# Kernel tuning notes

Hardware: AMD Instinct MI355X
Metric: run time of the kernel (lower is better)

## Reference

```python
import jax, jax.numpy as jnp
import numpy as np

B, L, DIM, H = 4, 2048, 768, 12
C = DIM // H  # head_dim = 64


def setup_inputs() -> dict:
    key = jax.random.key(0)
    k1, k2, k3 = jax.random.split(key, 3)
    x = jax.random.normal(k1, (B, L, DIM), dtype=jnp.float32)
    # qkv Linear: torch uniform init +-sqrt(6/(dim + 3*dim... per code: out//3 + in))
    val_qkv = np.sqrt(6.0 / float(DIM + DIM))
    Wqkv = jax.random.uniform(k2, (DIM, 3 * DIM), dtype=jnp.float32,
                              minval=-val_qkv, maxval=val_qkv)  # [in, out]
    # proj_out Linear: xavier uniform, bias zeros
    val_o = np.sqrt(6.0 / float(DIM + DIM))
    Wo = jax.random.uniform(k3, (DIM, DIM), dtype=jnp.float32,
                            minval=-val_o, maxval=val_o)  # [in, out]
    bo = jnp.zeros((DIM,), dtype=jnp.float32)
    return {"x": x, "Wqkv": Wqkv, "Wo": Wo, "bo": bo}


def reference(x, Wqkv, Wo, bo):
    b, l, d = x.shape
    qkv = x @ Wqkv                                   # [B, L, 3*dim] (qkv_bias=False)
    qkv = qkv.reshape(b, l, 3, H, C)                 # three interleaved as (three H C)
    q, k, v = qkv[:, :, 0], qkv[:, :, 1], qkv[:, :, 2]  # each [B, L, H, C]
    # NOTE: original forward never applies self.scale -> unscaled dot products
    dots = jnp.einsum('bqhc,bkhc->bhqk', q, k)       # [B, H, L, L]
    attn = jax.nn.softmax(dots, axis=-1)             # attn_drop = 0 -> identity
    out = jnp.einsum('bhqk,bkhc->bqhc', attn, v)     # [B, L, H, C]
    out = out.reshape(b, l, d)                       # (H C) -> dim
    return out @ Wo + bo                             # proj_drop = 0 -> identity
```

## Files before the change

kernel.cpp:

```cpp
#include <hip/hip_runtime.h>
#include <hip/hip_bf16.h>


typedef unsigned short u16;
typedef u16 u16x2 __attribute__((ext_vector_type(2)));
typedef u16 u16x4 __attribute__((ext_vector_type(4)));
typedef u16 u16x8 __attribute__((ext_vector_type(8)));
typedef short bf16x8 __attribute__((ext_vector_type(8)));
typedef float f32x4 __attribute__((ext_vector_type(4)));

#define MFMA16(acc, a, b) \
  asm("v_mfma_f32_16x16x32_bf16 %0, %1, %2, %0" : "+v"(acc) : "v"(a), "v"(b))

__device__ __forceinline__ u16 f2b(float f) {
  unsigned u = __float_as_uint(f);
  return (u16)((u + 0x7fffu + ((u >> 16) & 1u)) >> 16);
}
__device__ __forceinline__ float b2f(u16 h) {
  return __uint_as_float(((unsigned)h) << 16);
}
__device__ __forceinline__ unsigned pk_bf16(float a, float b) {
  unsigned d;
  asm("v_cvt_pk_bf16_f32 %0, %1, %2" : "=v"(d) : "v"(a), "v"(b));
  return d;
}

__device__ __forceinline__ void gload16(const u16* g, u16* l) {
  __builtin_amdgcn_global_load_lds(
      (const __attribute__((address_space(1))) unsigned*)g,
      (__attribute__((address_space(3))) unsigned*)l, 16, 0, 0);
}

__global__ __launch_bounds__(256) void prep_x_kernel(
    const float* __restrict__ X, u16* __restrict__ Xh, u16* __restrict__ Xl) {
  const size_t i = ((size_t)blockIdx.x * 256 + threadIdx.x) * 4;
  float4 v = *(const float4*)(X + i);
  u16 h0 = f2b(v.x), h1 = f2b(v.y), h2 = f2b(v.z), h3 = f2b(v.w);
  u16x4 hs = { h0, h1, h2, h3 };
  u16x4 ls = { f2b(v.x - b2f(h0)), f2b(v.y - b2f(h1)),
               f2b(v.z - b2f(h2)), f2b(v.w - b2f(h3)) };
  *(u16x4*)(Xh + i) = hs;
  *(u16x4*)(Xl + i) = ls;
}

__global__ __launch_bounds__(256) void prep_w_kernel(
    const float* __restrict__ W, u16* __restrict__ WtH, u16* __restrict__ WtL,
    int K, int N) {
  __shared__ float T[32][33];
  const int k0 = blockIdx.x * 32, n0 = blockIdx.y * 32;
  const int tx = threadIdx.x & 31, ty = threadIdx.x >> 5;
  #pragma unroll
  for (int i = 0; i < 4; ++i)
    T[ty + i * 8][tx] = W[(size_t)(k0 + ty + i * 8) * N + n0 + tx];
  __syncthreads();
  #pragma unroll
  for (int i = 0; i < 4; ++i) {
    const int rn = ty + i * 8, ck = tx;
    float v = T[ck][rn];
    u16 h = f2b(v);
    WtH[(size_t)(n0 + rn) * K + k0 + ck] = h;
    WtL[(size_t)(n0 + rn) * K + k0 + ck] = f2b(v - b2f(h));
  }
}

__global__ __launch_bounds__(256) void prep_wo_kernel(
    const float* __restrict__ W, u16* __restrict__ Wt, int K, int N) {
  __shared__ float T[32][33];
  const int k0 = blockIdx.x * 32, n0 = blockIdx.y * 32;
  const int tx = threadIdx.x & 31, ty = threadIdx.x >> 5;
  #pragma unroll
  for (int i = 0; i < 4; ++i)
    T[ty + i * 8][tx] = W[(size_t)(k0 + ty + i * 8) * N + n0 + tx];
  __syncthreads();
  #pragma unroll
  for (int i = 0; i < 4; ++i) {
    const int rn = ty + i * 8, ck = tx;
    Wt[(size_t)(n0 + rn) * K + k0 + ck] = f2b(T[ck][rn]);
  }
}

__global__ __launch_bounds__(256) void qkv_gemm_kernel(
    const u16* __restrict__ Xh, const u16* __restrict__ Xl,
    const u16* __restrict__ WtH, const u16* __restrict__ WtL,
    float* __restrict__ Qo, u16* __restrict__ Ko, u16* __restrict__ Vo) {
  __shared__ u16 Ah[4096], Al[4096], Bh[4096], Bl[4096];
  const int tid = threadIdx.x;
  const int w = tid >> 6, l = tid & 63;
  const int llo = l & 15, lhi = l >> 4;
  const int m0 = blockIdx.x * 128, n0 = blockIdx.y * 128;
  const int wr = (w >> 1) * 64, wc = (w & 1) * 64;

  f32x4 acc[4][4] = {};

  const int sr = tid >> 2;
  const int sc = (tid & 3) * 8;
  const unsigned lb = ((unsigned)w) * 512;
  const u16* axh = Xh + (size_t)(m0 + sr) * 768 + sc;
  const u16* axl = Xl + (size_t)(m0 + sr) * 768 + sc;
  const u16* bwh = WtH + (size_t)(n0 + sr) * 768 + sc;
  const u16* bwl = WtL + (size_t)(n0 + sr) * 768 + sc;
  const size_t half = (size_t)64 * 768;

  for (int k0 = 0; k0 < 768; k0 += 32) {
    __syncthreads();
    gload16(axh + k0,        Ah + lb);
    gload16(axh + half + k0, Ah + 2048 + lb);
    gload16(axl + k0,        Al + lb);
    gload16(axl + half + k0, Al + 2048 + lb);
    gload16(bwh + k0,        Bh + lb);
    gload16(bwh + half + k0, Bh + 2048 + lb);
    gload16(bwl + k0,        Bl + lb);
    gload16(bwl + half + k0, Bl + 2048 + lb);
    __syncthreads();
    bf16x8 ahf[4], alf[4], bhf[4], blf[4];
    #pragma unroll
    for (int i = 0; i < 4; ++i) {
      ahf[i] = *(const bf16x8*)&Ah[(wr + i * 16 + llo) * 32 + lhi * 8];
      alf[i] = *(const bf16x8*)&Al[(wr + i * 16 + llo) * 32 + lhi * 8];
    }
    #pragma unroll
    for (int n = 0; n < 4; ++n) {
      bhf[n] = *(const bf16x8*)&Bh[(wc + n * 16 + llo) * 32 + lhi * 8];
      blf[n] = *(const bf16x8*)&Bl[(wc + n * 16 + llo) * 32 + lhi * 8];
    }
    #pragma unroll
    for (int i = 0; i < 4; ++i)
      #pragma unroll
      for (int n = 0; n < 4; ++n) {
        MFMA16(acc[i][n], ahf[i], bhf[n]);
        MFMA16(acc[i][n], alf[i], bhf[n]);
        MFMA16(acc[i][n], ahf[i], blf[n]);
      }
  }

  const int t = n0 / 768;
  #pragma unroll
  for (int i = 0; i < 4; ++i) {
    #pragma unroll
    for (int n = 0; n < 4; ++n) {
      const int gc = n0 + wc + n * 16 + llo;
      const int rem = gc - t * 768;
      const int h = rem >> 6, c = rem & 63;
      #pragma unroll
      for (int r = 0; r < 4; ++r) {
        const int row = m0 + wr + i * 16 + lhi * 4 + r;
        const int b = row >> 11, lq = row & 2047;
        const size_t bh_ = (size_t)(b * 12 + h);
        const float fv = acc[i][n][r];
        if (t == 0)      Qo[(bh_ * 2048 + lq) * 64 + c] = fv;
        else if (t == 1) Ko[(bh_ * 2048 + lq) * 64 + c] = f2b(fv);
        else             Vo[(bh_ * 64 + c) * 2048 + lq] = f2b(fv);
      }
    }
  }
}

__global__ __launch_bounds__(256) void attn_kernel(
    const float* __restrict__ Qf, const u16* __restrict__ Km,
    const u16* __restrict__ Vt, u16* __restrict__ AO) {
  __shared__ u16 Ks[64][72];
  __shared__ u16 Vs[64][72];
  __shared__ u16 Ps[4][16][72];
  const int tid = threadIdx.x;
  const int w = tid >> 6, l = tid & 63;
  const int llo = l & 15, lhi = l >> 4;
  const int bh = blockIdx.y;
  const int q0 = blockIdx.x * 64 + w * 16;

  const float* Qp = Qf + ((size_t)bh * 2048 + q0 + llo) * 64 + lhi * 8;
  bf16x8 qf0h, qf0l, qf1h, qf1l;
  #pragma unroll
  for (int j = 0; j < 8; ++j) {
    float a = Qp[j], b = Qp[32 + j];
    u16 ha = f2b(a), hb = f2b(b);
    qf0h[j] = (short)ha; qf0l[j] = (short)f2b(a - b2f(ha));
    qf1h[j] = (short)hb; qf1l[j] = (short)f2b(b - b2f(hb));
  }

  const float L2E = 1.4426950408889634f;
  float mrow = -1e30f, lsum = 0.f;
  f32x4 o_acc[4] = {};

  for (int kt = 0; kt < 32; ++kt) {
    const int kb = kt * 64;
    __syncthreads();
    #pragma unroll
    for (int i = 0; i < 2; ++i) {
      const int idx = tid + i * 256;
      const int r = idx >> 3, ch = (idx & 7) * 8;
      *(u16x8*)&Ks[r][ch] = *(const u16x8*)(Km + ((size_t)bh * 2048 + kb + r) * 64 + ch);
      *(u16x8*)&Vs[r][ch] = *(const u16x8*)(Vt + ((size_t)bh * 64 + r) * 2048 + kb + ch);
    }
    __syncthreads();

    f32x4 s_acc[4] = {};
    #pragma unroll
    for (int kb4 = 0; kb4 < 4; ++kb4) {
      bf16x8 kf0 = *(const bf16x8*)&Ks[kb4 * 16 + llo][lhi * 8];
      bf16x8 kf1 = *(const bf16x8*)&Ks[kb4 * 16 + llo][32 + lhi * 8];
      MFMA16(s_acc[kb4], kf0, qf0h);
      MFMA16(s_acc[kb4], kf0, qf0l);
      MFMA16(s_acc[kb4], kf1, qf1h);
      MFMA16(s_acc[kb4], kf1, qf1l);
    }

    float tm01 = fmaxf(fmaxf(s_acc[0][0], s_acc[0][1]), fmaxf(s_acc[0][2], s_acc[0][3]));
    float tm23 = fmaxf(fmaxf(s_acc[1][0], s_acc[1][1]), fmaxf(s_acc[1][2], s_acc[1][3]));
    float tm45 = fmaxf(fmaxf(s_acc[2][0], s_acc[2][1]), fmaxf(s_acc[2][2], s_acc[2][3]));
    float tm67 = fmaxf(fmaxf(s_acc[3][0], s_acc[3][1]), fmaxf(s_acc[3][2], s_acc[3][3]));
    float tm = fmaxf(fmaxf(tm01, tm23), fmaxf(tm45, tm67));
    tm = fmaxf(tm, __shfl_xor(tm, 16));
    tm = fmaxf(tm, __shfl_xor(tm, 32));

    if (!__all(tm <= mrow + 8.f)) {
      const float mn = fmaxf(mrow, tm);
      const float scale = __expf(mrow - mn);
      mrow = mn;
      lsum *= scale;
      float scr[4];
      #pragma unroll
      for (int r = 0; r < 4; ++r) scr[r] = __shfl(scale, lhi * 20 + r);
      #pragma unroll
      for (int cb = 0; cb < 4; ++cb)
        #pragma unroll
        for (int r = 0; r < 4; ++r) o_acc[cb][r] *= scr[r];
    }

    const float mb = mrow * L2E;
    float rs = 0.f;
    #pragma unroll
    for (int kb4 = 0; kb4 < 4; ++kb4) {
      float p0 = exp2f(fmaf(s_acc[kb4][0], L2E, -mb));
      float p1 = exp2f(fmaf(s_acc[kb4][1], L2E, -mb));
      float p2 = exp2f(fmaf(s_acc[kb4][2], L2E, -mb));
      float p3 = exp2f(fmaf(s_acc[kb4][3], L2E, -mb));
      rs += (p0 + p1) + (p2 + p3);
      uint2 pk = { pk_bf16(p0, p1), pk_bf16(p2, p3) };
      *(uint2*)&Ps[w][llo][kb4 * 16 + lhi * 4] = pk;
    }
    rs += __shfl_xor(rs, 16);
    rs += __shfl_xor(rs, 32);
    lsum += rs;

    const bf16x8 pa0 = *(const bf16x8*)&Ps[w][llo][lhi * 8];
    const bf16x8 pa1 = *(const bf16x8*)&Ps[w][llo][32 + lhi * 8];
    #pragma unroll
    for (int cb = 0; cb < 4; ++cb) {
      bf16x8 vf0 = *(const bf16x8*)&Vs[cb * 16 + llo][lhi * 8];
      bf16x8 vf1 = *(const bf16x8*)&Vs[cb * 16 + llo][32 + lhi * 8];
      MFMA16(o_acc[cb], pa0, vf0);
      MFMA16(o_acc[cb], pa1, vf1);
    }
  }

  float ls[4];
  #pragma unroll
  for (int r = 0; r < 4; ++r) ls[r] = __shfl(lsum, lhi * 20 + r);
  const int b = bh / 12, h = bh % 12;
  #pragma unroll
  for (int cb = 0; cb < 4; ++cb)
    #pragma unroll
    for (int r = 0; r < 4; ++r) {
      const float val = o_acc[cb][r] / ls[r];
      AO[((size_t)(b * 2048 + q0 + lhi * 4 + r)) * 768 + h * 64 + cb * 16 + llo] = f2b(val);
    }
}

__global__ __launch_bounds__(256) void out_gemm_kernel(
    const u16* __restrict__ A, const u16* __restrict__ Wot,
    const float* __restrict__ bias, float* __restrict__ Out) {
  __shared__ u16 As[4096], Bs[4096];
  const int tid = threadIdx.x;
  const int w = tid >> 6, l = tid & 63;
  const int llo = l & 15, lhi = l >> 4;
  const int m0 = blockIdx.x * 128, n0 = blockIdx.y * 128;
  const int wr = (w >> 1) * 64, wc = (w & 1) * 64;

  f32x4 acc[4][4] = {};

  const int sr = tid >> 2;
  const int sc = (tid & 3) * 8;
  const unsigned lb = ((unsigned)w) * 512;
  const u16* ap = A   + (size_t)(m0 + sr) * 768 + sc;
  const u16* bp = Wot + (size_t)(n0 + sr) * 768 + sc;
  const size_t half = (size_t)64 * 768;

  for (int k0 = 0; k0 < 768; k0 += 32) {
    __syncthreads();
    gload16(ap + k0,        As + lb);
    gload16(ap + half + k0, As + 2048 + lb);
    gload16(bp + k0,        Bs + lb);
    gload16(bp + half + k0, Bs + 2048 + lb);
    __syncthreads();
    bf16x8 af[4], bfr[4];
    #pragma unroll
    for (int i = 0; i < 4; ++i)
      af[i] = *(const bf16x8*)&As[(wr + i * 16 + llo) * 32 + lhi * 8];
    #pragma unroll
    for (int n = 0; n < 4; ++n)
      bfr[n] = *(const bf16x8*)&Bs[(wc + n * 16 + llo) * 32 + lhi * 8];
    #pragma unroll
    for (int i = 0; i < 4; ++i)
      #pragma unroll
      for (int n = 0; n < 4; ++n)
        MFMA16(acc[i][n], af[i], bfr[n]);
  }

  #pragma unroll
  for (int i = 0; i < 4; ++i)
    #pragma unroll
    for (int n = 0; n < 4; ++n) {
      const int gc = n0 + wc + n * 16 + llo;
      const float bb = bias[gc];
      #pragma unroll
      for (int r = 0; r < 4; ++r) {
        const int row = m0 + wr + i * 16 + lhi * 4 + r;
        Out[(size_t)row * 768 + gc] = acc[i][n][r] + bb;
      }
    }
}

extern "C" void kernel_launch(void* const* d_in, const int* in_sizes, int n_in,
                              void* d_out, int out_size, void* d_ws, size_t ws_size,
                              hipStream_t stream) {
  const float* x    = (const float*)d_in[0];
  const float* Wqkv = (const float*)d_in[1];
  const float* Wo   = (const float*)d_in[2];
  const float* bo   = (const float*)d_in[3];
  float* out = (float*)d_out;

  const size_t SEG = (size_t)48 * 2048 * 64;
  float* qf  = (float*)d_ws;
  u16* kk    = (u16*)(qf + SEG);
  u16* vt    = kk + SEG;
  u16* xh    = vt + SEG;
  u16* xl    = xh + SEG;
  u16* wth   = xl + SEG;
  u16* wtl   = wth + (size_t)2304 * 768;
  u16* wot   = wtl + (size_t)2304 * 768;
  u16* ao    = xh;

  prep_x_kernel <<<dim3(6144), 256, 0, stream>>>(x, xh, xl);
  prep_w_kernel <<<dim3(24, 72), 256, 0, stream>>>(Wqkv, wth, wtl, 768, 2304);
  prep_wo_kernel<<<dim3(24, 24), 256, 0, stream>>>(Wo, wot, 768, 768);
  qkv_gemm_kernel<<<dim3(64, 18), 256, 0, stream>>>(xh, xl, wth, wtl, qf, kk, vt);
  attn_kernel   <<<dim3(32, 48), 256, 0, stream>>>(qf, kk, vt, ao);
  out_gemm_kernel<<<dim3(64, 6), 256, 0, stream>>>(ao, wot, bo, out);
}
```

Before: 271.5 us.

## Double-buffer K/V tiles and double attention block to 128 queries

The attention kernel now runs 512 threads (8 waves) per block over 128 query rows, so each K/V tile loaded into shared memory is reused by twice as many waves. K/V tiles are double-buffered: the next tile is fetched from global memory into registers while the current tile is computed, then written to the alternate buffer, which cuts one barrier per iteration. This uses more LDS per block and more registers for the prefetched values, and halves the grid size.

```diff
diff --git a/kernel.cpp b/kernel.cpp
--- a/kernel.cpp
+++ b/kernel.cpp
@@ -155,17 +155,21 @@
   }
 }
 
-__global__ __launch_bounds__(256) void attn_kernel(
+__global__ __launch_bounds__(512, 4) void attn_kernel(
     const float* __restrict__ Qf, const u16* __restrict__ Km,
     const u16* __restrict__ Vt, u16* __restrict__ AO) {
-  __shared__ u16 Ks[64][72];
-  __shared__ u16 Vs[64][72];
-  __shared__ u16 Ps[4][16][72];
+  __shared__ u16 Ks[2][64][72];
+  __shared__ u16 Vs[2][64][72];
+  __shared__ u16 Ps[8][16][72];
   const int tid = threadIdx.x;
   const int w = tid >> 6, l = tid & 63;
   const int llo = l & 15, lhi = l >> 4;
   const int bh = blockIdx.y;
-  const int q0 = blockIdx.x * 64 + w * 16;
+  const int q0 = blockIdx.x * 128 + w * 16;
+
+  const int kr = tid >> 3, ch = (tid & 7) * 8;
+  const u16* Kp = Km + ((size_t)bh * 2048 + kr) * 64 + ch;
+  const u16* Vp = Vt + ((size_t)bh * 64 + kr) * 2048 + ch;
 
   const float* Qp = Qf + ((size_t)bh * 2048 + q0 + llo) * 64 + lhi * 8;
   bf16x8 qf0h, qf0l, qf1h, qf1l;
@@ -181,23 +185,27 @@
   float mrow = -1e30f, lsum = 0.f;
   f32x4 o_acc[4] = {};
 
+  {
+    u16x8 nk = *(const u16x8*)(Kp);
+    u16x8 nv = *(const u16x8*)(Vp);
+    *(u16x8*)&Ks[0][kr][ch] = nk;
+    *(u16x8*)&Vs[0][kr][ch] = nv;
+  }
+  __syncthreads();
+
   for (int kt = 0; kt < 32; ++kt) {
-    const int kb = kt * 64;
-    __syncthreads();
-    #pragma unroll
-    for (int i = 0; i < 2; ++i) {
-      const int idx = tid + i * 256;
-      const int r = idx >> 3, ch = (idx & 7) * 8;
-      *(u16x8*)&Ks[r][ch] = *(const u16x8*)(Km + ((size_t)bh * 2048 + kb + r) * 64 + ch);
-      *(u16x8*)&Vs[r][ch] = *(const u16x8*)(Vt + ((size_t)bh * 64 + r) * 2048 + kb + ch);
-    }
-    __syncthreads();
+    const int cur = kt & 1;
+    u16x8 nk, nv;
+    if (kt < 31) {
+      nk = *(const u16x8*)(Kp + (size_t)(kt + 1) * 64 * 64);
+      nv = *(const u16x8*)(Vp + (size_t)(kt + 1) * 64);
+    }
 
     f32x4 s_acc[4] = {};
     #pragma unroll
     for (int kb4 = 0; kb4 < 4; ++kb4) {
-      bf16x8 kf0 = *(const bf16x8*)&Ks[kb4 * 16 + llo][lhi * 8];
-      bf16x8 kf1 = *(const bf16x8*)&Ks[kb4 * 16 + llo][32 + lhi * 8];
+      bf16x8 kf0 = *(const bf16x8*)&Ks[cur][kb4 * 16 + llo][lhi * 8];
+      bf16x8 kf1 = *(const bf16x8*)&Ks[cur][kb4 * 16 + llo][32 + lhi * 8];
       MFMA16(s_acc[kb4], kf0, qf0h);
       MFMA16(s_acc[kb4], kf0, qf0l);
       MFMA16(s_acc[kb4], kf1, qf1h);
@@ -246,11 +254,17 @@
     const bf16x8 pa1 = *(const bf16x8*)&Ps[w][llo][32 + lhi * 8];
     #pragma unroll
     for (int cb = 0; cb < 4; ++cb) {
-      bf16x8 vf0 = *(const bf16x8*)&Vs[cb * 16 + llo][lhi * 8];
-      bf16x8 vf1 = *(const bf16x8*)&Vs[cb * 16 + llo][32 + lhi * 8];
+      bf16x8 vf0 = *(const bf16x8*)&Vs[cur][cb * 16 + llo][lhi * 8];
+      bf16x8 vf1 = *(const bf16x8*)&Vs[cur][cb * 16 + llo][32 + lhi * 8];
       MFMA16(o_acc[cb], pa0, vf0);
       MFMA16(o_acc[cb], pa1, vf1);
     }
+
+    if (kt < 31) {
+      *(u16x8*)&Ks[cur ^ 1][kr][ch] = nk;
+      *(u16x8*)&Vs[cur ^ 1][kr][ch] = nv;
+    }
+    __syncthreads();
   }
 
   float ls[4];
@@ -344,6 +358,6 @@
   prep_w_kernel <<<dim3(24, 72), 256, 0, stream>>>(Wqkv, wth, wtl, 768, 2304);
   prep_wo_kernel<<<dim3(24, 24), 256, 0, stream>>>(Wo, wot, 768, 768);
   qkv_gemm_kernel<<<dim3(64, 18), 256, 0, stream>>>(xh, xl, wth, wtl, qf, kk, vt);
-  attn_kernel   <<<dim3(32, 48), 256, 0, stream>>>(qf, kk, vt, ao);
+  attn_kernel   <<<dim3(16, 48), 512, 0, stream>>>(qf, kk, vt, ao);
   out_gemm_kernel<<<dim3(64, 6), 256, 0, stream>>>(ao, wot, bo, out);
 }
```

Result: faster. 258.3 us (-4.9%).

## Double query rows per attention wave, prefetch K/V in registers, swizzle block order

Applied to the files above, without the earlier changes.

Each attention wave now handles 32 query rows as two 16-row slabs, so every K/V tile loaded into LDS feeds twice the MFMA work and the grid is halved. The next K/V tile is loaded into registers while the current tile is being computed, then written to LDS between barriers. Row-sum shuffles are deferred to the epilogue, and the max reduction runs only when a rescale is needed. Block indices in the attention kernel and both GEMMs are remapped with an XCD-style swizzle for cache locality, at the cost of more registers and fewer, larger blocks.

```diff
diff --git a/kernel.cpp b/kernel.cpp
--- a/kernel.cpp
+++ b/kernel.cpp
@@ -87,7 +87,9 @@
   const int tid = threadIdx.x;
   const int w = tid >> 6, l = tid & 63;
   const int llo = l & 15, lhi = l >> 4;
-  const int m0 = blockIdx.x * 128, n0 = blockIdx.y * 128;
+  const int id0 = blockIdx.y * 64 + blockIdx.x;
+  const int swz = (id0 & 7) * 144 + (id0 >> 3);
+  const int m0 = (swz & 63) * 128, n0 = (swz >> 6) * 128;
   const int wr = (w >> 1) * 64, wc = (w & 1) * 64;
 
   f32x4 acc[4][4] = {};
@@ -155,115 +157,161 @@
   }
 }
 
-__global__ __launch_bounds__(256) void attn_kernel(
+__global__ __launch_bounds__(256, 3) void attn_kernel(
     const float* __restrict__ Qf, const u16* __restrict__ Km,
     const u16* __restrict__ Vt, u16* __restrict__ AO) {
   __shared__ u16 Ks[64][72];
   __shared__ u16 Vs[64][72];
-  __shared__ u16 Ps[4][16][72];
+  __shared__ u16 Ps[4][32][72];
   const int tid = threadIdx.x;
   const int w = tid >> 6, l = tid & 63;
   const int llo = l & 15, lhi = l >> 4;
-  const int bh = blockIdx.y;
-  const int q0 = blockIdx.x * 64 + w * 16;
-
-  const float* Qp = Qf + ((size_t)bh * 2048 + q0 + llo) * 64 + lhi * 8;
-  bf16x8 qf0h, qf0l, qf1h, qf1l;
-  #pragma unroll
-  for (int j = 0; j < 8; ++j) {
-    float a = Qp[j], b = Qp[32 + j];
-    u16 ha = f2b(a), hb = f2b(b);
-    qf0h[j] = (short)ha; qf0l[j] = (short)f2b(a - b2f(ha));
-    qf1h[j] = (short)hb; qf1l[j] = (short)f2b(b - b2f(hb));
+  const int id0 = blockIdx.y * 16 + blockIdx.x;
+  const int swz = (id0 & 7) * 96 + (id0 >> 3);
+  const int bh = swz >> 4;
+  const int q0w = (swz & 15) * 128 + w * 32;
+
+  const int kr = tid >> 2, chs = (tid & 3) * 16;
+  const u16* Kp = Km + ((size_t)bh * 2048 + kr) * 64 + chs;
+  const u16* Vp = Vt + ((size_t)bh * 64 + kr) * 2048 + chs;
+
+  bf16x8 qh[2][2], ql[2][2];
+  #pragma unroll
+  for (int s = 0; s < 2; ++s) {
+    const float* Qp = Qf + ((size_t)bh * 2048 + q0w + s * 16 + llo) * 64 + lhi * 8;
+    #pragma unroll
+    for (int j = 0; j < 8; ++j) {
+      float a = Qp[j], b = Qp[32 + j];
+      u16 ha = f2b(a), hb = f2b(b);
+      qh[s][0][j] = (short)ha; ql[s][0][j] = (short)f2b(a - b2f(ha));
+      qh[s][1][j] = (short)hb; ql[s][1][j] = (short)f2b(b - b2f(hb));
+    }
   }
 
   const float L2E = 1.4426950408889634f;
-  float mrow = -1e30f, lsum = 0.f;
-  f32x4 o_acc[4] = {};
+  float mrow[2] = { -1e30f, -1e30f };
+  float lsum[2] = { 0.f, 0.f };
+  f32x4 o_acc[2][4] = {};
+
+  {
+    u16x8 k0 = *(const u16x8*)(Kp),     k1 = *(const u16x8*)(Kp + 8);
+    u16x8 v0 = *(const u16x8*)(Vp),     v1 = *(const u16x8*)(Vp + 8);
+    *(u16x8*)&Ks[kr][chs] = k0;  *(u16x8*)&Ks[kr][chs + 8] = k1;
+    *(u16x8*)&Vs[kr][chs] = v0;  *(u16x8*)&Vs[kr][chs + 8] = v1;
+  }
+  __syncthreads();
 
   for (int kt = 0; kt < 32; ++kt) {
-    const int kb = kt * 64;
-    __syncthreads();
-    #pragma unroll
-    for (int i = 0; i < 2; ++i) {
-      const int idx = tid + i * 256;
-      const int r = idx >> 3, ch = (idx & 7) * 8;
-      *(u16x8*)&Ks[r][ch] = *(const u16x8*)(Km + ((size_t)bh * 2048 + kb + r) * 64 + ch);
-      *(u16x8*)&Vs[r][ch] = *(const u16x8*)(Vt + ((size_t)bh * 64 + r) * 2048 + kb + ch);
-    }
-    __syncthreads();
-
-    f32x4 s_acc[4] = {};
+    u16x8 nk0, nk1, nv0, nv1;
+    if (kt < 31) {
+      const u16* kp = Kp + (size_t)(kt + 1) * 4096;
+      const u16* vp = Vp + (size_t)(kt + 1) * 64;
+      nk0 = *(const u16x8*)(kp);      nk1 = *(const u16x8*)(kp + 8);
+      nv0 = *(const u16x8*)(vp);      nv1 = *(const u16x8*)(vp + 8);
+    }
+
+    f32x4 s_acc[2][4] = {};
     #pragma unroll
     for (int kb4 = 0; kb4 < 4; ++kb4) {
       bf16x8 kf0 = *(const bf16x8*)&Ks[kb4 * 16 + llo][lhi * 8];
       bf16x8 kf1 = *(const bf16x8*)&Ks[kb4 * 16 + llo][32 + lhi * 8];
-      MFMA16(s_acc[kb4], kf0, qf0h);
-      MFMA16(s_acc[kb4], kf0, qf0l);
-      MFMA16(s_acc[kb4], kf1, qf1h);
-      MFMA16(s_acc[kb4], kf1, qf1l);
-    }
-
-    float tm01 = fmaxf(fmaxf(s_acc[0][0], s_acc[0][1]), fmaxf(s_acc[0][2], s_acc[0][3]));
-    float tm23 = fmaxf(fmaxf(s_acc[1][0], s_acc[1][1]), fmaxf(s_acc[1][2], s_acc[1][3]));
-    float tm45 = fmaxf(fmaxf(s_acc[2][0], s_acc[2][1]), fmaxf(s_acc[2][2], s_acc[2][3]));
-    float tm67 = fmaxf(fmaxf(s_acc[3][0], s_acc[3][1]), fmaxf(s_acc[3][2], s_acc[3][3]));
-    float tm = fmaxf(fmaxf(tm01, tm23), fmaxf(tm45, tm67));
-    tm = fmaxf(tm, __shfl_xor(tm, 16));
-    tm = fmaxf(tm, __shfl_xor(tm, 32));
-
-    if (!__all(tm <= mrow + 8.f)) {
-      const float mn = fmaxf(mrow, tm);
-      const float scale = __expf(mrow - mn);
-      mrow = mn;
-      lsum *= scale;
-      float scr[4];
-      #pragma unroll
-      for (int r = 0; r < 4; ++r) scr[r] = __shfl(scale, lhi * 20 + r);
-      #pragma unroll
-      for (int cb = 0; cb < 4; ++cb)
+      #pragma unroll
+      for (int s = 0; s < 2; ++s) {
+        MFMA16(s_acc[s][kb4], kf0, qh[s][0]);
+        MFMA16(s_acc[s][kb4], kf0, ql[s][0]);
+        MFMA16(s_acc[s][kb4], kf1, qh[s][1]);
+        MFMA16(s_acc[s][kb4], kf1, ql[s][1]);
+      }
+    }
+
+    float tm[2];
+    #pragma unroll
+    for (int s = 0; s < 2; ++s) {
+      float a = fmaxf(fmaxf(s_acc[s][0][0], s_acc[s][0][1]), fmaxf(s_acc[s][0][2], s_acc[s][0][3]));
+      float b = fmaxf(fmaxf(s_acc[s][1][0], s_acc[s][1][1]), fmaxf(s_acc[s][1][2], s_acc[s][1][3]));
+      float c = fmaxf(fmaxf(s_acc[s][2][0], s_acc[s][2][1]), fmaxf(s_acc[s][2][2], s_acc[s][2][3]));
+      float d = fmaxf(fmaxf(s_acc[s][3][0], s_acc[s][3][1]), fmaxf(s_acc[s][3][2], s_acc[s][3][3]));
+      tm[s] = fmaxf(fmaxf(a, b), fmaxf(c, d));
+    }
+
+    if (!__all(tm[0] <= mrow[0] + 8.f && tm[1] <= mrow[1] + 8.f)) {
+      #pragma unroll
+      for (int s = 0; s < 2; ++s) {
+        float g = tm[s];
+        g = fmaxf(g, __shfl_xor(g, 16));
+        g = fmaxf(g, __shfl_xor(g, 32));
+        const float mn = fmaxf(mrow[s], g);
+        const float scale = __expf(mrow[s] - mn);
+        mrow[s] = mn;
+        lsum[s] *= scale;
+        float scr[4];
         #pragma unroll
-        for (int r = 0; r < 4; ++r) o_acc[cb][r] *= scr[r];
-    }
-
-    const float mb = mrow * L2E;
-    float rs = 0.f;
-    #pragma unroll
-    for (int kb4 = 0; kb4 < 4; ++kb4) {
-      float p0 = exp2f(fmaf(s_acc[kb4][0], L2E, -mb));
-      float p1 = exp2f(fmaf(s_acc[kb4][1], L2E, -mb));
-      float p2 = exp2f(fmaf(s_acc[kb4][2], L2E, -mb));
-      float p3 = exp2f(fmaf(s_acc[kb4][3], L2E, -mb));
-      rs += (p0 + p1) + (p2 + p3);
-      uint2 pk = { pk_bf16(p0, p1), pk_bf16(p2, p3) };
-      *(uint2*)&Ps[w][llo][kb4 * 16 + lhi * 4] = pk;
-    }
-    rs += __shfl_xor(rs, 16);
-    rs += __shfl_xor(rs, 32);
-    lsum += rs;
-
-    const bf16x8 pa0 = *(const bf16x8*)&Ps[w][llo][lhi * 8];
-    const bf16x8 pa1 = *(const bf16x8*)&Ps[w][llo][32 + lhi * 8];
+        for (int r = 0; r < 4; ++r) scr[r] = __shfl(scale, lhi * 20 + r);
+        #pragma unroll
+        for (int cb = 0; cb < 4; ++cb)
+          #pragma unroll
+          for (int r = 0; r < 4; ++r) o_acc[s][cb][r] *= scr[r];
+      }
+    }
+
+    #pragma unroll
+    for (int s = 0; s < 2; ++s) {
+      const float mb = mrow[s] * L2E;
+      float rs = 0.f;
+      #pragma unroll
+      for (int kb4 = 0; kb4 < 4; ++kb4) {
+        float p0 = exp2f(fmaf(s_acc[s][kb4][0], L2E, -mb));
+        float p1 = exp2f(fmaf(s_acc[s][kb4][1], L2E, -mb));
+        float p2 = exp2f(fmaf(s_acc[s][kb4][2], L2E, -mb));
+        float p3 = exp2f(fmaf(s_acc[s][kb4][3], L2E, -mb));
+        rs += (p0 + p1) + (p2 + p3);
+        uint2 pk = { pk_bf16(p0, p1), pk_bf16(p2, p3) };
+        *(uint2*)&Ps[w][s * 16 + llo][kb4 * 16 + lhi * 4] = pk;
+      }
+      lsum[s] += rs;
+    }
+
+    bf16x8 pa[2][2];
+    #pragma unroll
+    for (int s = 0; s < 2; ++s) {
+      pa[s][0] = *(const bf16x8*)&Ps[w][s * 16 + llo][lhi * 8];
+      pa[s][1] = *(const bf16x8*)&Ps[w][s * 16 + llo][32 + lhi * 8];
+    }
     #pragma unroll
     for (int cb = 0; cb < 4; ++cb) {
       bf16x8 vf0 = *(const bf16x8*)&Vs[cb * 16 + llo][lhi * 8];
       bf16x8 vf1 = *(const bf16x8*)&Vs[cb * 16 + llo][32 + lhi * 8];
-      MFMA16(o_acc[cb], pa0, vf0);
-      MFMA16(o_acc[cb], pa1, vf1);
-    }
-  }
-
-  float ls[4];
-  #pragma unroll
-  for (int r = 0; r < 4; ++r) ls[r] = __shfl(lsum, lhi * 20 + r);
+      #pragma unroll
+      for (int s = 0; s < 2; ++s) {
+        MFMA16(o_acc[s][cb], pa[s][0], vf0);
+        MFMA16(o_acc[s][cb], pa[s][1], vf1);
+      }
+    }
+
+    __syncthreads();
+    if (kt < 31) {
+      *(u16x8*)&Ks[kr][chs] = nk0;  *(u16x8*)&Ks[kr][chs + 8] = nk1;
+      *(u16x8*)&Vs[kr][chs] = nv0;  *(u16x8*)&Vs[kr][chs + 8] = nv1;
+    }
+    __syncthreads();
+  }
+
   const int b = bh / 12, h = bh % 12;
   #pragma unroll
-  for (int cb = 0; cb < 4; ++cb)
-    #pragma unroll
-    for (int r = 0; r < 4; ++r) {
-      const float val = o_acc[cb][r] / ls[r];
-      AO[((size_t)(b * 2048 + q0 + lhi * 4 + r)) * 768 + h * 64 + cb * 16 + llo] = f2b(val);
-    }
+  for (int s = 0; s < 2; ++s) {
+    lsum[s] += __shfl_xor(lsum[s], 16);
+    lsum[s] += __shfl_xor(lsum[s], 32);
+    float ls[4];
+    #pragma unroll
+    for (int r = 0; r < 4; ++r) ls[r] = __shfl(lsum[s], lhi * 20 + r);
+    #pragma unroll
+    for (int cb = 0; cb < 4; ++cb)
+      #pragma unroll
+      for (int r = 0; r < 4; ++r) {
+        const float val = o_acc[s][cb][r] / ls[r];
+        AO[((size_t)(b * 2048 + q0w + s * 16 + lhi * 4 + r)) * 768 + h * 64 + cb * 16 + llo] = f2b(val);
+      }
+  }
 }
 
 __global__ __launch_bounds__(256) void out_gemm_kernel(
@@ -273,7 +321,9 @@
   const int tid = threadIdx.x;
   const int w = tid >> 6, l = tid & 63;
   const int llo = l & 15, lhi = l >> 4;
-  const int m0 = blockIdx.x * 128, n0 = blockIdx.y * 128;
+  const int id0 = blockIdx.y * 64 + blockIdx.x;
+  const int swz = (id0 & 7) * 48 + (id0 >> 3);
+  const int m0 = (swz & 63) * 128, n0 = (swz >> 6) * 128;
   const int wr = (w >> 1) * 64, wc = (w & 1) * 64;
 
   f32x4 acc[4][4] = {};
@@ -344,6 +394,6 @@
   prep_w_kernel <<<dim3(24, 72), 256, 0, stream>>>(Wqkv, wth, wtl, 768, 2304);
   prep_wo_kernel<<<dim3(24, 24), 256, 0, stream>>>(Wo, wot, 768, 768);
   qkv_gemm_kernel<<<dim3(64, 18), 256, 0, stream>>>(xh, xl, wth, wtl, qf, kk, vt);
-  attn_kernel   <<<dim3(32, 48), 256, 0, stream>>>(qf, kk, vt, ao);
+  attn_kernel   <<<dim3(16, 48), 256, 0, stream>>>(qf, kk, vt, ao);
   out_gemm_kernel<<<dim3(64, 6), 256, 0, stream>>>(ao, wot, bo, out);
 }
```

Result: no change. 276.7 us (+1.9%).
